# Optimization experiments

Measured on AMD Instinct MI355X. Metric: run time of the kernel, lower is better.

Reference implementation:

```python
import jax, jax.numpy as jnp
import numpy as np

DIM = 1024
N_HEADS = 16
HEAD_DIM = DIM // N_HEADS
SCALE = HEAD_DIM ** -0.5


def setup_inputs() -> dict:
    key = jax.random.key(0)
    ks = jax.random.split(key, 5)
    B, N = 2, 2048
    x = jax.random.normal(ks[0], (B, N, DIM), dtype=jnp.float32)
    # torch Linear: y = x @ W.T + b, W shape (out, in)
    qkv_w = jax.random.normal(ks[1], (3 * DIM, DIM), dtype=jnp.float32) * (DIM ** -0.5)
    qkv_b = jax.random.normal(ks[2], (3 * DIM,), dtype=jnp.float32) * 0.02
    proj_w = jax.random.normal(ks[3], (DIM, DIM), dtype=jnp.float32) * (DIM ** -0.5)
    proj_b = jax.random.normal(ks[4], (DIM,), dtype=jnp.float32) * 0.02
    return {"x": x, "qkv_w": qkv_w, "qkv_b": qkv_b, "proj_w": proj_w, "proj_b": proj_b}


def reference(x, qkv_w, qkv_b, proj_w, proj_b):
    B, N, D = x.shape
    qkv = x @ qkv_w.T + qkv_b                      # [B, N, 3D]
    qkv = qkv.reshape(B, N, 3, N_HEADS, HEAD_DIM)
    qkv = jnp.transpose(qkv, (2, 0, 3, 1, 4))      # [3, B, H, N, hd]
    q, k, v = qkv[0], qkv[1], qkv[2]
    dp = jnp.einsum('bhqd,bhkd->bhqk', q, k) * SCALE  # [B, H, N, N]
    attn = jax.nn.softmax(dp, axis=-1)
    wa = jnp.einsum('bhqk,bhkd->bhqd', attn, v)    # [B, H, N, hd]
    wa = jnp.transpose(wa, (0, 2, 1, 3)).reshape(B, N, D)
    return wa @ proj_w.T + proj_b
```

## Files before the change

### kernel.cpp

```cpp
#include <hip/hip_runtime.h>

#define BATCH 2
#define SEQ   2048
#define DIM   1024
#define NHEAD 16
#define HD    64
#define BH    (BATCH * NHEAD)
#define SCALE 0.125f
#define LOG2E 1.44269504f
#define NT    (SEQ / 64)

typedef __attribute__((ext_vector_type(8))) short short8;
typedef __attribute__((ext_vector_type(4))) float f32x4;

#define MFMA16(a, b, c) __builtin_amdgcn_mfma_f32_16x16x32_bf16(a, b, c, 0, 0, 0)

__device__ __forceinline__ ushort f2bf(float f) {
    union { float f; unsigned u; } v;
    v.f = f;
    unsigned r = (v.u + 0x7FFF + ((v.u >> 16) & 1)) >> 16;
    return (ushort)r;
}

__device__ __forceinline__ uint4 ld8f_bf16(const float* p) {
    float4 f0 = *(const float4*)p;
    float4 f1 = *(const float4*)(p + 4);
    union { ushort us[8]; uint4 v; } u;
    u.us[0] = f2bf(f0.x); u.us[1] = f2bf(f0.y);
    u.us[2] = f2bf(f0.z); u.us[3] = f2bf(f0.w);
    u.us[4] = f2bf(f1.x); u.us[5] = f2bf(f1.y);
    u.us[6] = f2bf(f1.z); u.us[7] = f2bf(f1.w);
    return u.v;
}

__device__ __forceinline__ void gl_lds16(const ushort* g, ushort* l) {
    __builtin_amdgcn_global_load_lds(
        (const __attribute__((address_space(1))) unsigned int*)g,
        (__attribute__((address_space(3))) unsigned int*)l,
        16, 0, 0);
}

#define N_X  (BATCH * SEQ * DIM)
#define N_QW (3 * DIM * DIM)
#define N_PW (DIM * DIM)

__global__ __launch_bounds__(256) void cvt_kernel(
    const float* __restrict__ x, const float* __restrict__ qw,
    const float* __restrict__ pw, ushort* __restrict__ xb,
    ushort* __restrict__ qwb, ushort* __restrict__ pwb)
{
    const int i = (blockIdx.x * 256 + threadIdx.x) * 8;
    if (i < N_X)  *(uint4*)(xb  + i) = ld8f_bf16(x  + i);
    if (i < N_QW) *(uint4*)(qwb + i) = ld8f_bf16(qw + i);
    if (i < N_PW) *(uint4*)(pwb + i) = ld8f_bf16(pw + i);
}

template <int MODE, typename TOUT>
__global__ __launch_bounds__(256, 2) void gemm_bt(
    const ushort* __restrict__ A, const ushort* __restrict__ W,
    const float* __restrict__ bias, TOUT* __restrict__ out,
    int M, int Nout, int K)
{
    __shared__ __align__(16) ushort As[128 * 32];
    __shared__ __align__(16) ushort Bs[128 * 32];

    const int tid  = threadIdx.x;
    const int wave = tid >> 6, lane = tid & 63;
    const int quad = lane >> 4, l16 = lane & 15;
    const int wm = wave >> 1, wn = wave & 1;
    const int m0 = blockIdx.y * 128, n0 = blockIdx.x * 128;

    const int c0 = tid, c1 = tid + 256;
    const ushort* gA0 = A + (size_t)(m0 + (c0 >> 2)) * K + (c0 & 3) * 8;
    const ushort* gA1 = A + (size_t)(m0 + (c1 >> 2)) * K + (c1 & 3) * 8;
    const ushort* gB0 = W + (size_t)(n0 + (c0 >> 2)) * K + (c0 & 3) * 8;
    const ushort* gB1 = W + (size_t)(n0 + (c1 >> 2)) * K + (c1 & 3) * 8;
    ushort* lA0 = &As[(wave * 64) * 8];
    ushort* lA1 = &As[(wave * 64 + 256) * 8];
    ushort* lB0 = &Bs[(wave * 64) * 8];
    ushort* lB1 = &Bs[(wave * 64 + 256) * 8];

    f32x4 acc[4][4];
#pragma unroll
    for (int i = 0; i < 4; i++)
#pragma unroll
        for (int j = 0; j < 4; j++) acc[i][j] = (f32x4){0.f, 0.f, 0.f, 0.f};

    for (int k0 = 0; k0 < K; k0 += 32) {
        gl_lds16(gA0 + k0, lA0);
        gl_lds16(gA1 + k0, lA1);
        gl_lds16(gB0 + k0, lB0);
        gl_lds16(gB1 + k0, lB1);
        __syncthreads();

        short8 af[4], bfr[4];
#pragma unroll
        for (int mt = 0; mt < 4; mt++)
            af[mt] = *(const short8*)&As[(wm * 64 + mt * 16 + l16) * 32 + quad * 8];
#pragma unroll
        for (int nt = 0; nt < 4; nt++)
            bfr[nt] = *(const short8*)&Bs[(wn * 64 + nt * 16 + l16) * 32 + quad * 8];
#pragma unroll
        for (int mt = 0; mt < 4; mt++)
#pragma unroll
            for (int nt = 0; nt < 4; nt++)
                acc[mt][nt] = MFMA16(af[mt], bfr[nt], acc[mt][nt]);
        __syncthreads();
    }

#pragma unroll
    for (int nt = 0; nt < 4; nt++) {
        const int n = n0 + wn * 64 + nt * 16 + l16;
        const float bv = bias[n];
#pragma unroll
        for (int mt = 0; mt < 4; mt++) {
            const int mBase = m0 + wm * 64 + mt * 16 + quad * 4;
#pragma unroll
            for (int r = 0; r < 4; r++) {
                const int m = mBase + r;
                float v = acc[mt][nt][r] + bv;
                if (MODE == 0) {
                    const int which = n >> 10, rem = n & 1023;
                    const int h = rem >> 6, d = rem & 63;
                    const int b = m >> 11, nq = m & 2047;
                    const int bh = b * NHEAD + h;
                    if (which == 0) v *= (SCALE * LOG2E);
                    size_t idx;
                    if (which == 2)
                        idx = (size_t)2 * BH * SEQ * HD + ((size_t)bh * HD + d) * SEQ + nq;
                    else
                        idx = (size_t)which * BH * SEQ * HD + ((size_t)bh * SEQ + nq) * HD + d;
                    ((ushort*)out)[idx] = f2bf(v);
                } else {
                    ((float*)out)[(size_t)m * Nout + n] = v;
                }
            }
        }
    }
}

#define PSTR 72

__global__ __launch_bounds__(256, 2) void attn_kernel(
    const ushort* __restrict__ qkv, ushort* __restrict__ wa)
{
    __shared__ __align__(16) ushort Ks[2][64 * 64];
    __shared__ __align__(16) ushort Vs[2][64 * 64];
    __shared__ __align__(16) ushort Pb[4][32 * PSTR];

    const int tid  = threadIdx.x;
    const int wave = tid >> 6, lane = tid & 63;
    const int quad = lane >> 4, l16 = lane & 15;
    const int bh = blockIdx.y;
    const int b = bh >> 4, h = bh & 15;
    const size_t hOff = (size_t)bh * SEQ * HD;
    const ushort* Q  = qkv + hOff;
    const ushort* Kg = qkv + (size_t)BH * SEQ * HD + hOff;
    const ushort* Vt = qkv + (size_t)2 * BH * SEQ * HD + hOff;
    const int q0 = blockIdx.x * 128 + wave * 32;

    short8 aq[2][2];
#pragma unroll
    for (int mt = 0; mt < 2; mt++)
#pragma unroll
        for (int kh = 0; kh < 2; kh++)
            aq[mt][kh] = *(const short8*)&Q[(size_t)(q0 + mt * 16 + l16) * HD + kh * 32 + quad * 8];

    f32x4 o[2][4];
#pragma unroll
    for (int mt = 0; mt < 2; mt++)
#pragma unroll
        for (int dt = 0; dt < 4; dt++) o[mt][dt] = (f32x4){0.f, 0.f, 0.f, 0.f};
    float lsum[2][4];
#pragma unroll
    for (int mt = 0; mt < 2; mt++)
#pragma unroll
        for (int r = 0; r < 4; r++) lsum[mt][r] = 0.f;

    ushort* Pw = &Pb[wave][0];

    const int rr = lane >> 3;
    const int cc = ((lane & 7) ^ rr) * 8;
    const ushort* KgL = Kg + rr * HD + cc;
    const ushort* VtL = Vt + (size_t)rr * SEQ + cc;

#define STAGE(buf, kt)                                                       \
    {                                                                        \
        _Pragma("unroll")                                                    \
        for (int jj = 0; jj < 2; jj++) {                                     \
            const int j = wave * 2 + jj;                                     \
            gl_lds16(KgL + (size_t)((kt) * 64 + j * 8) * HD,                 \
                     &Ks[buf][j * 512]);                                     \
            gl_lds16(VtL + (size_t)(j * 8) * SEQ + (kt) * 64,                \
                     &Vs[buf][j * 512]);                                     \
        }                                                                    \
    }

    STAGE(0, 0)

    const int sw  = (l16 & 7);
    const int ko0 = (quad ^ sw) * 8;
    const int ko1 = ko0 ^ 32;

    for (int kt = 0; kt < NT; kt++) {
        const int cur = kt & 1;
        __syncthreads();
        if (kt + 1 < NT) STAGE(cur ^ 1, kt + 1)

        f32x4 s[2][4];
#pragma unroll
        for (int t = 0; t < 4; t++) {
            const ushort* kb = &Ks[cur][(t * 16 + l16) * 64];
            short8 bk0 = *(const short8*)&kb[ko0];
            short8 bk1 = *(const short8*)&kb[ko1];
#pragma unroll
            for (int mt = 0; mt < 2; mt++) {
                f32x4 z = (f32x4){0.f, 0.f, 0.f, 0.f};
                z = MFMA16(aq[mt][0], bk0, z);
                z = MFMA16(aq[mt][1], bk1, z);
                s[mt][t] = z;
            }
        }

#pragma unroll
        for (int mt = 0; mt < 2; mt++)
#pragma unroll
            for (int t = 0; t < 4; t++)
#pragma unroll
                for (int r = 0; r < 4; r++) {
                    const float pv = __builtin_amdgcn_exp2f(s[mt][t][r]);
                    s[mt][t][r] = pv;
                    lsum[mt][r] += pv;
                }

        short8 bv[4][2];
#pragma unroll
        for (int dt = 0; dt < 4; dt++) {
            const ushort* vb = &Vs[cur][(dt * 16 + l16) * 64];
            bv[dt][0] = *(const short8*)&vb[ko0];
            bv[dt][1] = *(const short8*)&vb[ko1];
        }

        __builtin_amdgcn_fence(__ATOMIC_ACQ_REL, "workgroup");
#pragma unroll
        for (int mt = 0; mt < 2; mt++)
#pragma unroll
            for (int t = 0; t < 4; t++)
#pragma unroll
                for (int r = 0; r < 4; r++)
                    Pw[(mt * 16 + quad * 4 + r) * PSTR + l16 + t * 16] = f2bf(s[mt][t][r]);
        __builtin_amdgcn_fence(__ATOMIC_ACQ_REL, "workgroup");

        short8 pa[2][2];
#pragma unroll
        for (int mt = 0; mt < 2; mt++) {
            pa[mt][0] = *(const short8*)&Pw[(mt * 16 + l16) * PSTR + quad * 8];
            pa[mt][1] = *(const short8*)&Pw[(mt * 16 + l16) * PSTR + 32 + quad * 8];
        }

#pragma unroll
        for (int mt = 0; mt < 2; mt++)
#pragma unroll
            for (int dt = 0; dt < 4; dt++) {
                o[mt][dt] = MFMA16(pa[mt][0], bv[dt][0], o[mt][dt]);
                o[mt][dt] = MFMA16(pa[mt][1], bv[dt][1], o[mt][dt]);
            }
    }

#pragma unroll
    for (int mt = 0; mt < 2; mt++)
#pragma unroll
        for (int r = 0; r < 4; r++) {
            float ssum = lsum[mt][r];
            ssum += __shfl_xor(ssum, 1);
            ssum += __shfl_xor(ssum, 2);
            ssum += __shfl_xor(ssum, 4);
            ssum += __shfl_xor(ssum, 8);
            lsum[mt][r] = ssum;
        }

#pragma unroll
    for (int mt = 0; mt < 2; mt++)
#pragma unroll
        for (int r = 0; r < 4; r++) {
            const float inv = 1.f / lsum[mt][r];
            const int qrow = q0 + mt * 16 + quad * 4 + r;
            ushort* dst = wa + ((size_t)(b * SEQ + qrow)) * DIM + h * HD;
#pragma unroll
            for (int dt = 0; dt < 4; dt++)
                dst[dt * 16 + l16] = f2bf(o[mt][dt][r] * inv);
        }
}

extern "C" void kernel_launch(void* const* d_in, const int* in_sizes, int n_in,
                              void* d_out, int out_size, void* d_ws, size_t ws_size,
                              hipStream_t stream)
{
    const float* x      = (const float*)d_in[0];
    const float* qkv_w  = (const float*)d_in[1];
    const float* qkv_b  = (const float*)d_in[2];
    const float* proj_w = (const float*)d_in[3];
    const float* proj_b = (const float*)d_in[4];
    float* out = (float*)d_out;

    ushort* xb  = (ushort*)d_ws;
    ushort* qwb = xb  + (size_t)N_X;
    ushort* pwb = qwb + (size_t)N_QW;
    ushort* qkv = pwb + (size_t)N_PW;
    ushort* wa  = qkv + (size_t)3 * BH * SEQ * HD;

    const int M = BATCH * SEQ;
    dim3 blk(256);

    cvt_kernel<<<dim3((N_X / 8 + 255) / 256), blk, 0, stream>>>(
        x, qkv_w, proj_w, xb, qwb, pwb);

    gemm_bt<0, ushort><<<dim3((3 * DIM) / 128, M / 128), blk, 0, stream>>>(
        xb, qwb, qkv_b, qkv, M, 3 * DIM, DIM);

    attn_kernel<<<dim3(SEQ / 128, BH), blk, 0, stream>>>(qkv, wa);

    gemm_bt<1, float><<<dim3(DIM / 128, M / 128), blk, 0, stream>>>(
        wa, pwb, proj_b, out, M, DIM, DIM);
}
```

Measured before the change: 209.7 us.

## Double-buffer GEMM LDS tiles and use 64-row tiles for projection GEMM

The GEMM kernel now holds two LDS buffers per operand and issues the global-to-LDS loads for the next K tile before computing on the current one. This replaces the two barriers per iteration with a single one and overlaps loads with MFMA work. The kernel is also templated on the M tile size, and the output projection uses 64-row tiles so its grid has twice as many blocks to fill the CUs. LDS use per block doubles, which may reduce occupancy, and the smaller tile lowers data reuse in the projection GEMM.

```diff
diff --git a/kernel.cpp b/kernel.cpp
--- a/kernel.cpp
+++ b/kernel.cpp
@@ -55,57 +55,62 @@
     if (i < N_PW) *(uint4*)(pwb + i) = ld8f_bf16(pw + i);
 }
 
-template <int MODE, typename TOUT>
+template <int MODE, int WM, typename TOUT>
 __global__ __launch_bounds__(256, 2) void gemm_bt(
     const ushort* __restrict__ A, const ushort* __restrict__ W,
     const float* __restrict__ bias, TOUT* __restrict__ out,
     int M, int Nout, int K)
 {
-    __shared__ __align__(16) ushort As[128 * 32];
-    __shared__ __align__(16) ushort Bs[128 * 32];
+    constexpr int BM = 2 * WM * 16;
+    __shared__ __align__(16) ushort As[2][BM * 32];
+    __shared__ __align__(16) ushort Bs[2][128 * 32];
 
     const int tid  = threadIdx.x;
     const int wave = tid >> 6, lane = tid & 63;
     const int quad = lane >> 4, l16 = lane & 15;
     const int wm = wave >> 1, wn = wave & 1;
-    const int m0 = blockIdx.y * 128, n0 = blockIdx.x * 128;
+    const int m0 = blockIdx.y * BM, n0 = blockIdx.x * 128;
 
     const int c0 = tid, c1 = tid + 256;
     const ushort* gA0 = A + (size_t)(m0 + (c0 >> 2)) * K + (c0 & 3) * 8;
     const ushort* gA1 = A + (size_t)(m0 + (c1 >> 2)) * K + (c1 & 3) * 8;
     const ushort* gB0 = W + (size_t)(n0 + (c0 >> 2)) * K + (c0 & 3) * 8;
     const ushort* gB1 = W + (size_t)(n0 + (c1 >> 2)) * K + (c1 & 3) * 8;
-    ushort* lA0 = &As[(wave * 64) * 8];
-    ushort* lA1 = &As[(wave * 64 + 256) * 8];
-    ushort* lB0 = &Bs[(wave * 64) * 8];
-    ushort* lB1 = &Bs[(wave * 64 + 256) * 8];
-
-    f32x4 acc[4][4];
-#pragma unroll
-    for (int i = 0; i < 4; i++)
+
+#define STAGE_G(buf, k0)                                                  \
+    {                                                                     \
+        gl_lds16(gA0 + (k0), &As[buf][(wave * 64) * 8]);                  \
+        if (WM == 4) gl_lds16(gA1 + (k0), &As[buf][(wave * 64 + 256) * 8]); \
+        gl_lds16(gB0 + (k0), &Bs[buf][(wave * 64) * 8]);                  \
+        gl_lds16(gB1 + (k0), &Bs[buf][(wave * 64 + 256) * 8]);            \
+    }
+
+    f32x4 acc[WM][4];
+#pragma unroll
+    for (int i = 0; i < WM; i++)
 #pragma unroll
         for (int j = 0; j < 4; j++) acc[i][j] = (f32x4){0.f, 0.f, 0.f, 0.f};
 
-    for (int k0 = 0; k0 < K; k0 += 32) {
-        gl_lds16(gA0 + k0, lA0);
-        gl_lds16(gA1 + k0, lA1);
-        gl_lds16(gB0 + k0, lB0);
-        gl_lds16(gB1 + k0, lB1);
+    const int KT = K >> 5;
+    STAGE_G(0, 0)
+
+    for (int kt = 0; kt < KT; kt++) {
+        const int cur = kt & 1;
         __syncthreads();
-
-        short8 af[4], bfr[4];
-#pragma unroll
-        for (int mt = 0; mt < 4; mt++)
-            af[mt] = *(const short8*)&As[(wm * 64 + mt * 16 + l16) * 32 + quad * 8];
+        if (kt + 1 < KT) STAGE_G(cur ^ 1, (kt + 1) * 32)
+
+        short8 af[WM], bfr[4];
+#pragma unroll
+        for (int mt = 0; mt < WM; mt++)
+            af[mt] = *(const short8*)&As[cur][(wm * (WM * 16) + mt * 16 + l16) * 32 + quad * 8];
 #pragma unroll
         for (int nt = 0; nt < 4; nt++)
-            bfr[nt] = *(const short8*)&Bs[(wn * 64 + nt * 16 + l16) * 32 + quad * 8];
-#pragma unroll
-        for (int mt = 0; mt < 4; mt++)
+            bfr[nt] = *(const short8*)&Bs[cur][(wn * 64 + nt * 16 + l16) * 32 + quad * 8];
+#pragma unroll
+        for (int mt = 0; mt < WM; mt++)
 #pragma unroll
             for (int nt = 0; nt < 4; nt++)
                 acc[mt][nt] = MFMA16(af[mt], bfr[nt], acc[mt][nt]);
-        __syncthreads();
     }
 
 #pragma unroll
@@ -113,8 +118,8 @@
         const int n = n0 + wn * 64 + nt * 16 + l16;
         const float bv = bias[n];
 #pragma unroll
-        for (int mt = 0; mt < 4; mt++) {
-            const int mBase = m0 + wm * 64 + mt * 16 + quad * 4;
+        for (int mt = 0; mt < WM; mt++) {
+            const int mBase = m0 + wm * (WM * 16) + mt * 16 + quad * 4;
 #pragma unroll
             for (int r = 0; r < 4; r++) {
                 const int m = mBase + r;
@@ -137,6 +142,7 @@
             }
         }
     }
+#undef STAGE_G
 }
 
 #define PSTR 72
@@ -315,11 +321,11 @@
     cvt_kernel<<<dim3((N_X / 8 + 255) / 256), blk, 0, stream>>>(
         x, qkv_w, proj_w, xb, qwb, pwb);
 
-    gemm_bt<0, ushort><<<dim3((3 * DIM) / 128, M / 128), blk, 0, stream>>>(
+    gemm_bt<0, 4, ushort><<<dim3((3 * DIM) / 128, M / 128), blk, 0, stream>>>(
         xb, qwb, qkv_b, qkv, M, 3 * DIM, DIM);
 
     attn_kernel<<<dim3(SEQ / 128, BH), blk, 0, stream>>>(qkv, wa);
 
-    gemm_bt<1, float><<<dim3(DIM / 128, M / 128), blk, 0, stream>>>(
+    gemm_bt<1, 2, float><<<dim3(DIM / 128, M / 64), blk, 0, stream>>>(
         wa, pwb, proj_b, out, M, DIM, DIM);
 }
```

Result: no change. 206.1 us (-1.7%).
